# Kernel optimization log

Measured on AMD Instinct MI355X. Metric: run time of the kernel, lower is better.

## Reference

```python
import jax, jax.numpy as jnp
import numpy as np

TAU = 1.0  # FLAGS.tau


def setup_inputs() -> dict:
    key = jax.random.key(0)
    k1, k2, k3, k4 = jax.random.split(key, 4)
    B, N, E, D_in, D_out = 64, 512, 8, 64, 64
    edge_features = jax.random.normal(k1, (B, N, N, E), dtype=jnp.float32)
    x = jax.random.normal(k2, (B * N, D_in), dtype=jnp.float32)
    # glorot init for weights, normal for coef (as in source)
    lim = np.sqrt(6.0 / (D_in + D_out))
    W = jax.random.uniform(k3, (D_in, D_out), dtype=jnp.float32, minval=-lim, maxval=lim)
    coef = jax.random.normal(k4, (E, 1), dtype=jnp.float32)
    return {"edge_features": edge_features, "x": x, "W": W, "coef": coef}


def reference(edge_features, x, W, coef):
    B, N, _, E = edge_features.shape
    D_out = W.shape[1]
    # node transform: [B*N, D_in] @ [D_in, D_out]
    pre_sup = (x @ W).reshape(B, N, D_out)
    # per-edge attention score: [B,N,N,E] @ [E,1] -> [B,N,N]
    scores = jnp.einsum('bije,e->bij', edge_features, coef[:, 0])
    adj = jax.nn.softmax(scores / TAU, axis=-1)
    # preprocess_adj: add self-loops, symmetric D^-1/2 (A+I) D^-1/2.
    # Block-diagonal structure means normalization is per-graph, so we stay batched
    # instead of materializing the [B*N, B*N] block-diagonal matrix.
    adj_hat = adj + jnp.eye(N, dtype=adj.dtype)
    d_inv_sqrt = jax.lax.rsqrt(adj_hat.sum(axis=-1))  # [B,N]
    adj_norm = adj_hat * d_inv_sqrt[:, :, None] * d_inv_sqrt[:, None, :]
    # adjacency-weighted aggregation (block-diagonal matmul == batched matmul)
    out = jnp.einsum('bij,bjd->bid', adj_norm, pre_sup).reshape(B * N, D_out)
    return jax.nn.relu(out)
```

## Files before the change

kernel.cpp:

```cpp
#include <hip/hip_runtime.h>
#include <hip/hip_bf16.h>
#include <math.h>

#define B_  64
#define N_  512
#define E_  8
#define D_  64
#define LDP 264

typedef float f32x4 __attribute__((ext_vector_type(4)));
typedef short s16x8 __attribute__((ext_vector_type(8)));
typedef unsigned short u16;
typedef unsigned int u32;

__device__ __forceinline__ u16 bf16_rne(float x) {
    u32 u = __float_as_uint(x);
    u = (u + 0x7fffu + ((u >> 16) & 1u)) >> 16;
    return (u16)u;
}


__global__ __launch_bounds__(256) void presup_kernel(
    const float* __restrict__ x, const float* __restrict__ W,
    float* __restrict__ ps, u16* __restrict__ psT)
{
    __shared__ float Wl[64 * 64];
    const int t = threadIdx.x;
#pragma unroll
    for (int i = 0; i < 4; ++i)
        ((f32x4*)Wl)[t + i * 256] = ((const f32x4*)W)[t + i * 256];
    __syncthreads();

    const int d4  = (t & 15) * 4;
    const int r   = t >> 4;
    const int row = blockIdx.x * 16 + r;
    const float* xr = x + (size_t)row * 64;

    f32x4 acc = 0.f;
#pragma unroll
    for (int k = 0; k < 64; k += 4) {
        f32x4 xv = *(const f32x4*)&xr[k];
        f32x4 w0 = *(const f32x4*)&Wl[(k + 0) * 64 + d4];
        f32x4 w1 = *(const f32x4*)&Wl[(k + 1) * 64 + d4];
        f32x4 w2 = *(const f32x4*)&Wl[(k + 2) * 64 + d4];
        f32x4 w3 = *(const f32x4*)&Wl[(k + 3) * 64 + d4];
        acc += xv.x * w0;
        acc += xv.y * w1;
        acc += xv.z * w2;
        acc += xv.w * w3;
    }
    *(f32x4*)&ps[(size_t)row * 64 + d4] = acc;

    const int b  = row >> 9, rb = row & 511;
#pragma unroll
    for (int i = 0; i < 4; ++i)
        psT[((size_t)b * 64 + d4 + i) * 512 + rb] = bf16_rne(acc[i]);
}

__global__ __launch_bounds__(256, 2) void fused_kernel(
    const float* __restrict__ edge, const float* __restrict__ coef,
    const u16* __restrict__ psT, const float* __restrict__ ps,
    float* __restrict__ out)
{
    __shared__ u16  pl[4][16][LDP];
    __shared__ float dn[4][16];

    const int t = threadIdx.x, w = t >> 6, l = t & 63;
    const int b  = blockIdx.x >> 3;
    const int i0 = (blockIdx.x & 7) * 64 + w * 16;
    const int ln = l & 15, g = l >> 4;

    f32x4 cA, cB;
    cA.x = coef[0]; cA.y = coef[1]; cA.z = coef[2]; cA.w = coef[3];
    cB.x = coef[4]; cB.y = coef[5]; cB.z = coef[6]; cB.w = coef[7];
    const f32x4 ch = (l & 1) ? cB : cA;

    const float* ebase = edge + ((size_t)b * N_ + i0) * (size_t)(N_ * E_) + 4 * l;
    const u16*   Ab    = psT + ((size_t)b * 64 + ln) * 512 + g * 8;

    f32x4 acc0 = {0.f,0.f,0.f,0.f}, acc1 = acc0, acc2 = acc0, acc3 = acc0;

#pragma unroll
    for (int h = 0; h < 2; ++h) {
        for (int r = 0; r < 16; ++r) {
            const float* rp = ebase + (size_t)r * (N_ * E_) + h * 2048;
            float ls = 0.f;
#pragma unroll
            for (int c2 = 0; c2 < 8; ++c2) {
                f32x4 e = *(const f32x4*)(rp + c2 * 256);
                float dd = e.x * ch.x + e.y * ch.y + e.z * ch.z + e.w * ch.w;
                dd += __shfl_xor(dd, 1, 64);
                float p = __expf(dd);
                ls += p;
                pl[w][r][c2 * 32 + (l >> 1)] = bf16_rne(p);
            }
#pragma unroll
            for (int off = 32; off; off >>= 1) ls += __shfl_xor(ls, off, 64);
            if (l == 0) dn[w][r] = (h == 0) ? ls : (dn[w][r] + ls);
        }

        s16x8 bf[8];
#pragma unroll
        for (int kk = 0; kk < 8; ++kk)
            bf[kk] = *(const s16x8*)&pl[w][ln][kk * 32 + g * 8];
#pragma unroll
        for (int kk = 0; kk < 8; ++kk) {
            const int ko = h * 256 + kk * 32;
            s16x8 a0 = *(const s16x8*)(Ab + (size_t)(0 * 16) * 512 + ko);
            s16x8 a1 = *(const s16x8*)(Ab + (size_t)(1 * 16) * 512 + ko);
            s16x8 a2 = *(const s16x8*)(Ab + (size_t)(2 * 16) * 512 + ko);
            s16x8 a3 = *(const s16x8*)(Ab + (size_t)(3 * 16) * 512 + ko);
            acc0 = __builtin_amdgcn_mfma_f32_16x16x32_bf16(a0, bf[kk], acc0, 0, 0, 0);
            acc1 = __builtin_amdgcn_mfma_f32_16x16x32_bf16(a1, bf[kk], acc1, 0, 0, 0);
            acc2 = __builtin_amdgcn_mfma_f32_16x16x32_bf16(a2, bf[kk], acc2, 0, 0, 0);
            acc3 = __builtin_amdgcn_mfma_f32_16x16x32_bf16(a3, bf[kk], acc3, 0, 0, 0);
        }
    }

    const float rs = 1.f / dn[w][ln];
    const int   i  = i0 + ln;
    const size_t rowoff = ((size_t)b * N_ + i) * 64;

#pragma unroll
    for (int mt = 0; mt < 4; ++mt) {
        f32x4 acc = (mt == 0) ? acc0 : (mt == 1) ? acc1 : (mt == 2) ? acc2 : acc3;
        const int d0 = mt * 16 + g * 4;
        f32x4 self = *(const f32x4*)&ps[rowoff + d0];
        f32x4 o;
#pragma unroll
        for (int c = 0; c < 4; ++c)
            o[c] = fmaxf(acc[c] * rs + 0.5f * self[c], 0.f);
        *(f32x4*)&out[rowoff + d0] = o;
    }
}

extern "C" void kernel_launch(void* const* d_in, const int* in_sizes, int n_in,
                              void* d_out, int out_size, void* d_ws, size_t ws_size,
                              hipStream_t stream) {
    const float* edge = (const float*)d_in[0];
    const float* x    = (const float*)d_in[1];
    const float* W    = (const float*)d_in[2];
    const float* coef = (const float*)d_in[3];
    float* out = (float*)d_out;

    char* ws = (char*)d_ws;
    float* ps  = (float*)ws;
    u16*   psT = (u16*)(ws + (8u << 20));

    presup_kernel<<<(B_ * N_) / 16, 256, 0, stream>>>(x, W, ps, psT);
    fused_kernel<<<B_ * 8, 256, 0, stream>>>(edge, coef, psT, ps, out);
}
```

Measured before the change: 130.5 us.

## Software-pipeline edge row loads four deep and use DPP for pair sum

The per-row edge loop is restructured into a software pipeline. Four register buffers of edge data are kept in flight, so global loads for later rows are issued before the current rows' softmax numerators are computed. The xor-1 shuffle is replaced by a DPP quad-perm move, avoiding an LDS-routed bpermute. The extra buffers raise register pressure (128 extra VGPRs for the buffers), which may hurt occupancy under launch_bounds(256,2).

```diff
diff --git a/kernel.cpp b/kernel.cpp
--- a/kernel.cpp
+++ b/kernel.cpp
@@ -17,6 +17,11 @@
     u32 u = __float_as_uint(x);
     u = (u + 0x7fffu + ((u >> 16) & 1u)) >> 16;
     return (u16)u;
+}
+
+__device__ __forceinline__ float pair_sum(float x) {
+    int y = __builtin_amdgcn_mov_dpp(__float_as_int(x), 0xB1, 0xF, 0xF, true);
+    return x + __int_as_float(y);
 }
 
 
@@ -80,25 +85,31 @@
 
     f32x4 acc0 = {0.f,0.f,0.f,0.f}, acc1 = acc0, acc2 = acc0, acc3 = acc0;
 
+    auto LOADC = [&](f32x4 (&buf)[8], int c) {
+        const float* rp = ebase + (size_t)(c & 15) * (N_ * E_) + (c >> 4) * 2048;
 #pragma unroll
-    for (int h = 0; h < 2; ++h) {
-        for (int r = 0; r < 16; ++r) {
-            const float* rp = ebase + (size_t)r * (N_ * E_) + h * 2048;
-            float ls = 0.f;
+        for (int c2 = 0; c2 < 8; ++c2)
+            buf[c2] = *(const f32x4*)(rp + c2 * 256);
+    };
+
+    auto COMPUTE = [&](const f32x4 (&buf)[8], int c) {
+        const int r = c & 15;
+        float ls = 0.f;
 #pragma unroll
-            for (int c2 = 0; c2 < 8; ++c2) {
-                f32x4 e = *(const f32x4*)(rp + c2 * 256);
-                float dd = e.x * ch.x + e.y * ch.y + e.z * ch.z + e.w * ch.w;
-                dd += __shfl_xor(dd, 1, 64);
-                float p = __expf(dd);
-                ls += p;
-                pl[w][r][c2 * 32 + (l >> 1)] = bf16_rne(p);
-            }
+        for (int c2 = 0; c2 < 8; ++c2) {
+            f32x4 e = buf[c2];
+            float dd = e.x * ch.x + e.y * ch.y + e.z * ch.z + e.w * ch.w;
+            dd = pair_sum(dd);
+            float p = __expf(dd);
+            ls += p;
+            pl[w][r][c2 * 32 + (l >> 1)] = bf16_rne(p);
+        }
 #pragma unroll
-            for (int off = 32; off; off >>= 1) ls += __shfl_xor(ls, off, 64);
-            if (l == 0) dn[w][r] = (h == 0) ? ls : (dn[w][r] + ls);
-        }
+        for (int off = 32; off; off >>= 1) ls += __shfl_xor(ls, off, 64);
+        if (l == 0) dn[w][r] = (c >> 4) ? (dn[w][r] + ls) : ls;
+    };
 
+    auto MFMA = [&](int h) {
         s16x8 bf[8];
 #pragma unroll
         for (int kk = 0; kk < 8; ++kk)
@@ -115,6 +126,18 @@
             acc2 = __builtin_amdgcn_mfma_f32_16x16x32_bf16(a2, bf[kk], acc2, 0, 0, 0);
             acc3 = __builtin_amdgcn_mfma_f32_16x16x32_bf16(a3, bf[kk], acc3, 0, 0, 0);
         }
+    };
+
+    f32x4 bA[8], bB[8], bC[8], bD[8];
+    LOADC(bA, 0); LOADC(bB, 1);
+    for (int c = 0; c < 32; c += 4) {
+        LOADC(bC, c + 2); LOADC(bD, c + 3);
+        COMPUTE(bA, c);
+        COMPUTE(bB, c + 1);
+        if (c + 4 < 32) { LOADC(bA, c + 4); LOADC(bB, c + 5); }
+        COMPUTE(bC, c + 2);
+        COMPUTE(bD, c + 3);
+        if ((c & 15) == 12) MFMA(c >> 4);
     }
 
     const float rs = 1.f / dn[w][ln];
@@ -128,8 +151,8 @@
         f32x4 self = *(const f32x4*)&ps[rowoff + d0];
         f32x4 o;
 #pragma unroll
-        for (int c = 0; c < 4; ++c)
-            o[c] = fmaxf(acc[c] * rs + 0.5f * self[c], 0.f);
+        for (int cc = 0; cc < 4; ++cc)
+            o[cc] = fmaxf(acc[cc] * rs + 0.5f * self[cc], 0.f);
         *(f32x4*)&out[rowoff + d0] = o;
     }
 }
```

After: 130.0 us. Within noise of the previous version (-0.4%).

## Split fused softmax-aggregation into separate score and MFMA aggregation kernels

Applied to the files above, without the earlier changes.

Splits the fused edge-scoring and aggregation kernel into two. A high-parallelism score kernel streams edge features with double-buffered loads and writes normalized bf16 probabilities. A separate kernel then runs the MFMA aggregation. The intent is to raise occupancy and memory-level parallelism on the dominant edge-tensor read. The cost is an extra intermediate probability matrix written to and read back from global memory, plus an additional launch.

```diff
diff --git a/kernel.cpp b/kernel.cpp
--- a/kernel.cpp
+++ b/kernel.cpp
@@ -6,7 +6,6 @@
 #define N_  512
 #define E_  8
 #define D_  64
-#define LDP 264
 
 typedef float f32x4 __attribute__((ext_vector_type(4)));
 typedef short s16x8 __attribute__((ext_vector_type(8)));
@@ -17,6 +16,11 @@
     u32 u = __float_as_uint(x);
     u = (u + 0x7fffu + ((u >> 16) & 1u)) >> 16;
     return (u16)u;
+}
+
+__device__ __forceinline__ float pair_sum(float x) {
+    int y = __builtin_amdgcn_mov_dpp(__float_as_int(x), 0xB1, 0xF, 0xF, true);
+    return x + __int_as_float(y);
 }
 
 
@@ -57,70 +61,90 @@
         psT[((size_t)b * 64 + d4 + i) * 512 + rb] = bf16_rne(acc[i]);
 }
 
-__global__ __launch_bounds__(256, 2) void fused_kernel(
+__global__ __launch_bounds__(256) void score_kernel(
     const float* __restrict__ edge, const float* __restrict__ coef,
-    const u16* __restrict__ psT, const float* __restrict__ ps,
-    float* __restrict__ out)
+    u16* __restrict__ Pn)
 {
-    __shared__ u16  pl[4][16][LDP];
-    __shared__ float dn[4][16];
-
     const int t = threadIdx.x, w = t >> 6, l = t & 63;
-    const int b  = blockIdx.x >> 3;
-    const int i0 = (blockIdx.x & 7) * 64 + w * 16;
-    const int ln = l & 15, g = l >> 4;
+    const size_t row = (size_t)blockIdx.x * 4 + w;
+    const float* eb = edge + row * (size_t)(N_ * E_) + 4 * l;
 
     f32x4 cA, cB;
     cA.x = coef[0]; cA.y = coef[1]; cA.z = coef[2]; cA.w = coef[3];
     cB.x = coef[4]; cB.y = coef[5]; cB.z = coef[6]; cB.w = coef[7];
     const f32x4 ch = (l & 1) ? cB : cA;
+    const int src = (2 * l) & 63;
 
-    const float* ebase = edge + ((size_t)b * N_ + i0) * (size_t)(N_ * E_) + 4 * l;
-    const u16*   Ab    = psT + ((size_t)b * 64 + ln) * 512 + g * 8;
+    f32x4 bA[4], bB[4];
+    float pk[16];
+    float lsum = 0.f;
+
+    auto LOAD = [&](f32x4 (&buf)[4], int g) {
+#pragma unroll
+        for (int k = 0; k < 4; ++k)
+            buf[k] = *(const f32x4*)(eb + (size_t)(g * 4 + k) * 256);
+    };
+    auto COMP = [&](const f32x4 (&buf)[4], int g) {
+#pragma unroll
+        for (int k = 0; k < 4; ++k) {
+            f32x4 e = buf[k];
+            float dd = e.x * ch.x + e.y * ch.y + e.z * ch.z + e.w * ch.w;
+            dd = pair_sum(dd);
+            float p = __expf(dd);
+            pk[g * 4 + k] = p;
+            lsum += p;
+        }
+    };
+
+    LOAD(bA, 0);
+    LOAD(bB, 1);
+    COMP(bA, 0);  LOAD(bA, 2);
+    COMP(bB, 1);  LOAD(bB, 3);
+    COMP(bA, 2);
+    COMP(bB, 3);
+
+#pragma unroll
+    for (int off = 32; off; off >>= 1) lsum += __shfl_xor(lsum, off, 64);
+    const float rs = 2.f / lsum;
+
+    u16* op = Pn + row * N_;
+#pragma unroll
+    for (int gg = 0; gg < 8; ++gg) {
+        float pa = __shfl(pk[2 * gg],     src, 64);
+        float pb = __shfl(pk[2 * gg + 1], src, 64);
+        float pv = (l < 32) ? pa : pb;
+        op[gg * 64 + l] = bf16_rne(pv * rs);
+    }
+}
+
+__global__ __launch_bounds__(256) void agg_kernel(
+    const u16* __restrict__ Pn, const u16* __restrict__ psT,
+    const float* __restrict__ ps, float* __restrict__ out)
+{
+    const int t = threadIdx.x, w = t >> 6, l = t & 63;
+    const int b  = blockIdx.x >> 3;
+    const int n0 = (blockIdx.x & 7) * 64 + w * 16;
+    const int ln = l & 15, g = l >> 4;
+
+    const u16* Ab = psT + ((size_t)b * 64 + ln) * 512 + g * 8;
+    const u16* Bb = Pn  + ((size_t)b * N_ + n0 + ln) * 512 + g * 8;
 
     f32x4 acc0 = {0.f,0.f,0.f,0.f}, acc1 = acc0, acc2 = acc0, acc3 = acc0;
-
 #pragma unroll
-    for (int h = 0; h < 2; ++h) {
-        for (int r = 0; r < 16; ++r) {
-            const float* rp = ebase + (size_t)r * (N_ * E_) + h * 2048;
-            float ls = 0.f;
-#pragma unroll
-            for (int c2 = 0; c2 < 8; ++c2) {
-                f32x4 e = *(const f32x4*)(rp + c2 * 256);
-                float dd = e.x * ch.x + e.y * ch.y + e.z * ch.z + e.w * ch.w;
-                dd += __shfl_xor(dd, 1, 64);
-                float p = __expf(dd);
-                ls += p;
-                pl[w][r][c2 * 32 + (l >> 1)] = bf16_rne(p);
-            }
-#pragma unroll
-            for (int off = 32; off; off >>= 1) ls += __shfl_xor(ls, off, 64);
-            if (l == 0) dn[w][r] = (h == 0) ? ls : (dn[w][r] + ls);
-        }
-
-        s16x8 bf[8];
-#pragma unroll
-        for (int kk = 0; kk < 8; ++kk)
-            bf[kk] = *(const s16x8*)&pl[w][ln][kk * 32 + g * 8];
-#pragma unroll
-        for (int kk = 0; kk < 8; ++kk) {
-            const int ko = h * 256 + kk * 32;
-            s16x8 a0 = *(const s16x8*)(Ab + (size_t)(0 * 16) * 512 + ko);
-            s16x8 a1 = *(const s16x8*)(Ab + (size_t)(1 * 16) * 512 + ko);
-            s16x8 a2 = *(const s16x8*)(Ab + (size_t)(2 * 16) * 512 + ko);
-            s16x8 a3 = *(const s16x8*)(Ab + (size_t)(3 * 16) * 512 + ko);
-            acc0 = __builtin_amdgcn_mfma_f32_16x16x32_bf16(a0, bf[kk], acc0, 0, 0, 0);
-            acc1 = __builtin_amdgcn_mfma_f32_16x16x32_bf16(a1, bf[kk], acc1, 0, 0, 0);
-            acc2 = __builtin_amdgcn_mfma_f32_16x16x32_bf16(a2, bf[kk], acc2, 0, 0, 0);
-            acc3 = __builtin_amdgcn_mfma_f32_16x16x32_bf16(a3, bf[kk], acc3, 0, 0, 0);
-        }
+    for (int k0 = 0; k0 < 512; k0 += 32) {
+        s16x8 bb = *(const s16x8*)(Bb + k0);
+        s16x8 a0 = *(const s16x8*)(Ab + (size_t)(0 * 16) * 512 + k0);
+        s16x8 a1 = *(const s16x8*)(Ab + (size_t)(1 * 16) * 512 + k0);
+        s16x8 a2 = *(const s16x8*)(Ab + (size_t)(2 * 16) * 512 + k0);
+        s16x8 a3 = *(const s16x8*)(Ab + (size_t)(3 * 16) * 512 + k0);
+        acc0 = __builtin_amdgcn_mfma_f32_16x16x32_bf16(a0, bb, acc0, 0, 0, 0);
+        acc1 = __builtin_amdgcn_mfma_f32_16x16x32_bf16(a1, bb, acc1, 0, 0, 0);
+        acc2 = __builtin_amdgcn_mfma_f32_16x16x32_bf16(a2, bb, acc2, 0, 0, 0);
+        acc3 = __builtin_amdgcn_mfma_f32_16x16x32_bf16(a3, bb, acc3, 0, 0, 0);
     }
 
-    const float rs = 1.f / dn[w][ln];
-    const int   i  = i0 + ln;
+    const int i = n0 + ln;
     const size_t rowoff = ((size_t)b * N_ + i) * 64;
-
 #pragma unroll
     for (int mt = 0; mt < 4; ++mt) {
         f32x4 acc = (mt == 0) ? acc0 : (mt == 1) ? acc1 : (mt == 2) ? acc2 : acc3;
@@ -128,8 +152,8 @@
         f32x4 self = *(const f32x4*)&ps[rowoff + d0];
         f32x4 o;
 #pragma unroll
-        for (int c = 0; c < 4; ++c)
-            o[c] = fmaxf(acc[c] * rs + 0.5f * self[c], 0.f);
+        for (int cc = 0; cc < 4; ++cc)
+            o[cc] = fmaxf(0.5f * (acc[cc] + self[cc]), 0.f);
         *(f32x4*)&out[rowoff + d0] = o;
     }
 }
@@ -146,7 +170,9 @@
     char* ws = (char*)d_ws;
     float* ps  = (float*)ws;
     u16*   psT = (u16*)(ws + (8u << 20));
+    u16*   Pn  = (u16*)(ws + (12u << 20));
 
     presup_kernel<<<(B_ * N_) / 16, 256, 0, stream>>>(x, W, ps, psT);
-    fused_kernel<<<B_ * 8, 256, 0, stream>>>(edge, coef, psT, ps, out);
+    score_kernel<<<(B_ * N_) / 4, 256, 0, stream>>>(edge, coef, Pn);
+    agg_kernel<<<B_ * 8, 256, 0, stream>>>(Pn, psT, ps, out);
 }
```

Result: slower. 149.1 us (+14.2%).
